# Optimization experiments

Hardware: AMD Instinct MI355X
Metric: run time of the kernel (lower is better)

The kernel has to match this reference:

```python
import jax, jax.numpy as jnp
import numpy as np

B = 4096
D = 512
N_I = 1000000
N_T = 1000000
GAMMA = 0.8
EPS = 1e-10
RHO_I = 8.0
RHO_T = 8.0
ETA_INIT = 1e-05
BETA_U = 0.5
GRAD_CLIP = 5.0
TAU_MIN, TAU_MAX = 0.005, 0.05
TAU_INIT = 0.01


def setup_inputs() -> dict:
    key = jax.random.key(0)
    k1, k2 = jax.random.split(key)
    img = jax.random.normal(k1, (B, D), jnp.float32)
    txt = jax.random.normal(k2, (B, D), jnp.float32)
    # CLIP-style L2-normalized features
    img = img / jnp.linalg.norm(img, axis=1, keepdims=True)
    txt = txt / jnp.linalg.norm(txt, axis=1, keepdims=True)
    return {
        "image_features": img,
        "text_features": txt,
        "s_I": jnp.zeros(N_I, jnp.float32),
        "s_T": jnp.zeros(N_T, jnp.float32),
        "b_I": jnp.zeros(N_I, jnp.float32),
        "b_T": jnp.zeros(N_T, jnp.float32),
        "u_I": jnp.zeros(N_I, jnp.float32),
        "u_T": jnp.zeros(N_T, jnp.float32),
        "tau_I": jnp.full((N_I,), TAU_INIT, jnp.float32),
        "tau_T": jnp.full((N_T,), TAU_INIT, jnp.float32),
        "image_ids": jnp.arange(B, dtype=jnp.int32),
        "text_ids": jnp.arange(B, dtype=jnp.int32),
        "epoch": 1,
    }


def reference(image_features, text_features, s_I, s_T, b_I, b_T, u_I, u_T,
              tau_I, tau_T, image_ids, text_ids, epoch):
    sg = jax.lax.stop_gradient
    sim = jnp.einsum('id,jd->ij', image_features, text_features)  # [B,B]
    diag = jnp.diagonal(sim)
    Bn = sim.shape[0]
    tau_img = tau_I[image_ids]  # [B]
    tau_txt = tau_T[text_ids]   # [B]
    image_diffs = sim - diag[:, None]
    text_diffs = sim - diag[None, :]
    # .detach() in the original -> stop_gradient here
    idt = sg(image_diffs / tau_img[:, None])
    tdt = sg(text_diffs / tau_txt[None, :])
    old_b_I = b_I[image_ids]
    old_b_T = b_T[text_ids]
    # running max for log-sum-exp stabilization
    b_I_row = jnp.maximum(idt.max(axis=1), old_b_I)
    b_T_col = jnp.maximum(tdt.max(axis=0), old_b_T)
    b_I_new = b_I.at[image_ids].set(b_I_row)
    b_T_new = b_T.at[text_ids].set(b_T_col)
    mask = 1.0 - jnp.eye(Bn, dtype=sim.dtype)
    exp_i = jnp.exp(idt - b_I_row[:, None]) * mask
    exp_t = jnp.exp(tdt - b_T_col[None, :]) * mask
    g_I = exp_i.sum(axis=1)
    g_T = exp_t.sum(axis=0)
    if epoch == 0:
        sI = g_I
        sT = g_T
    else:
        sI = (1.0 - GAMMA) * s_I[image_ids] * jnp.exp(old_b_I - b_I_row) + GAMMA * g_I
        sT = (1.0 - GAMMA) * s_T[text_ids] * jnp.exp(old_b_T - b_T_col) + GAMMA * g_T
    s_I_new = s_I.at[image_ids].set(sI)
    s_T_new = s_T.at[text_ids].set(sT)
    w_i = sg(exp_i / (sI[:, None] + EPS))
    w_t = sg(exp_t / (sT[None, :] + EPS))
    image_loss = (w_i * image_diffs).sum(axis=1)
    text_loss = (w_t * text_diffs).sum(axis=0)
    total_loss = image_loss.mean() + text_loss.mean()
    tw_i = jnp.log(sI / (Bn - 1)) + b_I_row + RHO_I - (w_i * idt).sum(axis=1)
    tw_t = jnp.log(sT / (Bn - 1)) + b_T_col + RHO_T - (w_t * tdt).sum(axis=0)
    # torch uses in-place clamp_ on a view, so the returned means are clipped
    tw_i = jnp.clip(tw_i, -GRAD_CLIP, GRAD_CLIP)
    tw_t = jnp.clip(tw_t, -GRAD_CLIP, GRAD_CLIP)
    u_I_val = (1.0 - BETA_U) * u_I[image_ids] + BETA_U * tw_i
    u_T_val = (1.0 - BETA_U) * u_T[text_ids] + BETA_U * tw_t
    u_I_new = u_I.at[image_ids].set(u_I_val)
    u_T_new = u_T.at[text_ids].set(u_T_val)
    tau_I_new = tau_I.at[image_ids].set(jnp.clip(tau_img - ETA_INIT * u_I_val, TAU_MIN, TAU_MAX))
    tau_T_new = tau_T.at[text_ids].set(jnp.clip(tau_txt - ETA_INIT * u_T_val, TAU_MIN, TAU_MAX))
    return (total_loss, tau_img.mean(), tau_txt.mean(), tw_i.mean(), tw_t.mean(),
            s_I_new, s_T_new, b_I_new, b_T_new, u_I_new, u_T_new, tau_I_new, tau_T_new)
```

## Files before the change

### kernel.cpp

```cpp
#include <hip/hip_runtime.h>

typedef unsigned short u16;
typedef unsigned int u32;

typedef __bf16 bf16x8 __attribute__((ext_vector_type(8)));
typedef float floatx4 __attribute__((ext_vector_type(4)));

__device__ __forceinline__ u16 f2bf(float f) {
    union { float f; u32 u; } c; c.f = f;
    u32 u = c.u;
    u32 r = u + 0x7FFFu + ((u >> 16) & 1u);
    return (u16)(r >> 16);
}
__device__ __forceinline__ float bf2f(u16 x) {
    union { u32 u; float f; } c; c.u = ((u32)x) << 16; return c.f;
}

__device__ __forceinline__ void comb(float& M, float& P0, float& P1,
                                     float m, float p0, float p1) {
    float nm = fmaxf(M, m);
    float s = __expf(M - nm), t = __expf(m - nm);
    P0 = P0 * s + p0 * t;
    P1 = P1 * s + p1 * t;
    M = nm;
}

__device__ __forceinline__ void dma16(const u16* g, u16* l) {
#if __has_builtin(__builtin_amdgcn_global_load_lds)
    __builtin_amdgcn_global_load_lds(
        (const __attribute__((address_space(1))) u32*)g,
        (__attribute__((address_space(3))) u32*)l, 16, 0, 0);
#else
    int lane = threadIdx.x & 63;
    *(uint4*)(l + lane * 8) = *(const uint4*)(g);
#endif
}

__global__ __launch_bounds__(256) void presplit(
    const float* __restrict__ a, const float* __restrict__ b,
    u16* __restrict__ Ah, u16* __restrict__ Al,
    u16* __restrict__ Bh, u16* __restrict__ Bl, int n,
    const float* __restrict__ tauI, const float* __restrict__ tauT,
    const int* __restrict__ img_ids, const int* __restrict__ txt_ids,
    float* __restrict__ taur, float* __restrict__ tauc) {
    if (blockIdx.y == 0 && blockIdx.x < 16) {
        int t = blockIdx.x * 256 + threadIdx.x;
        taur[t] = tauI[img_ids[t]];
        tauc[t] = tauT[txt_ids[t]];
    }
    const float* src = blockIdx.y ? b : a;
    u16* dh = blockIdx.y ? Bh : Ah;
    u16* dl = blockIdx.y ? Bl : Al;
    int i = (blockIdx.x * 256 + threadIdx.x) * 8;
    if (i >= n) return;
    float4 v0 = *(const float4*)&src[i];
    float4 v1 = *(const float4*)&src[i + 4];
    float xs[8] = {v0.x, v0.y, v0.z, v0.w, v1.x, v1.y, v1.z, v1.w};
    u16 h[8], l[8];
#pragma unroll
    for (int e = 0; e < 8; e++) {
        h[e] = f2bf(xs[e]);
        l[e] = f2bf(xs[e] - bf2f(h[e]));
    }
    *(uint4*)&dh[i] = *(uint4*)h;
    *(uint4*)&dl[i] = *(uint4*)l;
}

#define COPY_BLOCKS 2048

__global__ __launch_bounds__(256) void gemm_flash(
    const u16* __restrict__ Ah, const u16* __restrict__ Al,
    const u16* __restrict__ Bh, const u16* __restrict__ Bl,
    const float* __restrict__ taur, const float* __restrict__ tauc,
    float* __restrict__ rowpart, float* __restrict__ colpart,
    float* __restrict__ diag,
    const float* __restrict__ p0, const float* __restrict__ p1,
    const float* __restrict__ p2, const float* __restrict__ p3,
    const float* __restrict__ p4, const float* __restrict__ p5,
    const float* __restrict__ p6, const float* __restrict__ p7,
    float* __restrict__ out, long long n) {
    __shared__ __align__(16) u16 sAh[128 * 32];
    __shared__ __align__(16) u16 sAl[128 * 32];
    __shared__ __align__(16) u16 sBh[128 * 32];
    __shared__ __align__(16) u16 sBl[128 * 32];
    __shared__ float redbuf[1536];

    const int bid = blockIdx.x;
    if (bid >= 1024) {
        const int cb = bid - 1024;
        const float* srcs[8] = {p0, p1, p2, p3, p4, p5, p6, p7};
        const long long total = 8 * n;
        const long long G = (total - 3) >> 2;
        for (long long g = (long long)cb * 256 + threadIdx.x; g < G;
             g += (long long)COPY_BLOCKS * 256) {
            long long e = 3 + 4 * g;
            int k = (int)(e / n);
            long long bound = (long long)(k + 1) * n;
            float vv[4];
#pragma unroll
            for (int j = 0; j < 4; j++) {
                long long ee = e + j;
                int kk = (ee >= bound) ? k + 1 : k;
                vv[j] = srcs[kk][ee - (long long)kk * n];
            }
            float4 q = {vv[0], vv[1], vv[2], vv[3]};
            *(float4*)&out[5 + e] = q;
        }
        if (cb == 0) {
            int t = threadIdx.x;
            long long tail0 = 3 + 4 * G;
            int tcount = (int)(total - tail0);
            long long e = -1;
            if (t < 3) e = t;
            else if (t < 3 + tcount) e = tail0 + (t - 3);
            if (e >= 0) {
                int k = (int)(e / n);
                out[5 + e] = srcs[k][e - (long long)k * n];
            }
        }
        return;
    }

    const int tid  = threadIdx.x;
    const int wave = tid >> 6, lane = tid & 63;
    const int lr = lane & 15, quad = lane >> 4;
    const int waveM = wave >> 1, waveN = wave & 1;
    const int rowtile = bid >> 5, coltile = bid & 31;
    const int rowBase = rowtile * 128;
    const int colBase = coltile * 128;

    const int o0 = wave * 1024 + lane * 16;
    const int o1 = o0 + 4096;
    const int r0s = o0 >> 6, c0s = (o0 & 63) >> 1;
    const int r1s = o1 >> 6, c1s = (o1 & 63) >> 1;
    const int l0 = wave * 512;
    const int l1 = wave * 512 + 2048;

    floatx4 acc[4][4];
#pragma unroll
    for (int mi = 0; mi < 4; mi++)
#pragma unroll
        for (int ni = 0; ni < 4; ni++) acc[mi][ni] = (floatx4)0.0f;

    for (int k0 = 0; k0 < 512; k0 += 32) {
        __syncthreads();
        dma16(&Ah[(size_t)(rowBase + r0s) * 512 + k0 + c0s], sAh + l0);
        dma16(&Ah[(size_t)(rowBase + r1s) * 512 + k0 + c1s], sAh + l1);
        dma16(&Al[(size_t)(rowBase + r0s) * 512 + k0 + c0s], sAl + l0);
        dma16(&Al[(size_t)(rowBase + r1s) * 512 + k0 + c1s], sAl + l1);
        dma16(&Bh[(size_t)(colBase + r0s) * 512 + k0 + c0s], sBh + l0);
        dma16(&Bh[(size_t)(colBase + r1s) * 512 + k0 + c1s], sBh + l1);
        dma16(&Bl[(size_t)(colBase + r0s) * 512 + k0 + c0s], sBl + l0);
        dma16(&Bl[(size_t)(colBase + r1s) * 512 + k0 + c1s], sBl + l1);
        __syncthreads();

        bf16x8 afh[4], afl[4], bfh[4], bfl[4];
#pragma unroll
        for (int mi = 0; mi < 4; mi++) {
            int off = (waveM * 64 + mi * 16 + lr) * 32 + quad * 8;
            afh[mi] = *(const bf16x8*)&sAh[off];
            afl[mi] = *(const bf16x8*)&sAl[off];
        }
#pragma unroll
        for (int ni = 0; ni < 4; ni++) {
            int off = (waveN * 64 + ni * 16 + lr) * 32 + quad * 8;
            bfh[ni] = *(const bf16x8*)&sBh[off];
            bfl[ni] = *(const bf16x8*)&sBl[off];
        }
#pragma unroll
        for (int mi = 0; mi < 4; mi++)
#pragma unroll
            for (int ni = 0; ni < 4; ni++) {
                acc[mi][ni] = __builtin_amdgcn_mfma_f32_16x16x32_bf16(afh[mi], bfh[ni], acc[mi][ni], 0, 0, 0);
                acc[mi][ni] = __builtin_amdgcn_mfma_f32_16x16x32_bf16(afh[mi], bfl[ni], acc[mi][ni], 0, 0, 0);
                acc[mi][ni] = __builtin_amdgcn_mfma_f32_16x16x32_bf16(afl[mi], bfh[ni], acc[mi][ni], 0, 0, 0);
            }
    }


    if (rowtile == coltile && waveM == waveN) {
#pragma unroll
        for (int mi = 0; mi < 4; mi++)
#pragma unroll
            for (int r = 0; r < 4; r++)
                if (lr == quad * 4 + r)
                    diag[colBase + waveN * 64 + mi * 16 + lr] = acc[mi][mi][r];
    }

#pragma unroll
    for (int mi = 0; mi < 4; mi++) {
#pragma unroll
        for (int r = 0; r < 4; r++) {
            int row_local = waveM * 64 + mi * 16 + quad * 4 + r;
            float it = 1.0f / taur[rowBase + row_local];
            float M = -3.4e38f, P0 = 0.f, P1 = 0.f;
#pragma unroll
            for (int ni = 0; ni < 4; ni++) {
                float y = acc[mi][ni][r] * it;
                comb(M, P0, P1, y, 1.0f, y);
            }
#pragma unroll
            for (int mask = 1; mask <= 8; mask <<= 1) {
                float om = __shfl_xor(M, mask);
                float o0 = __shfl_xor(P0, mask);
                float o1 = __shfl_xor(P1, mask);
                comb(M, P0, P1, om, o0, o1);
            }
            if (lr == 0) {
                int x = (row_local * 2 + waveN) * 3;
                redbuf[x] = M; redbuf[x + 1] = P0; redbuf[x + 2] = P1;
            }
        }
    }

#pragma unroll
    for (int ni = 0; ni < 4; ni++) {
        int col_local = waveN * 64 + ni * 16 + lr;
        float it = 1.0f / tauc[colBase + col_local];
        float M = -3.4e38f, P0 = 0.f, P1 = 0.f;
#pragma unroll
        for (int mi = 0; mi < 4; mi++)
#pragma unroll
            for (int r = 0; r < 4; r++) {
                float y = acc[mi][ni][r] * it;
                comb(M, P0, P1, y, 1.0f, y);
            }
#pragma unroll
        for (int mask = 16; mask <= 32; mask <<= 1) {
            float om = __shfl_xor(M, mask);
            float o0 = __shfl_xor(P0, mask);
            float o1 = __shfl_xor(P1, mask);
            comb(M, P0, P1, om, o0, o1);
        }
        if (quad == 0) {
            int x = 768 + (col_local * 2 + waveM) * 3;
            redbuf[x] = M; redbuf[x + 1] = P0; redbuf[x + 2] = P1;
        }
    }
    __syncthreads();

    if (tid < 128) {
        int x = tid * 6;
        float M = redbuf[x], P0 = redbuf[x + 1], P1 = redbuf[x + 2];
        comb(M, P0, P1, redbuf[x + 3], redbuf[x + 4], redbuf[x + 5]);
        float* dst = &rowpart[(size_t)(rowBase + tid) * 96 + coltile * 3];
        dst[0] = M; dst[1] = P0; dst[2] = P1;
    } else {
        int c = tid - 128;
        int x = 768 + c * 6;
        float M = redbuf[x], P0 = redbuf[x + 1], P1 = redbuf[x + 2];
        comb(M, P0, P1, redbuf[x + 3], redbuf[x + 4], redbuf[x + 5]);
        float* dst = &colpart[(size_t)(colBase + c) * 96 + rowtile * 3];
        dst[0] = M; dst[1] = P0; dst[2] = P1;
    }
}

struct FinArgs {
    const float* rowpart; const float* colpart; const float* diag;
    const float* tauI; const float* sI; const float* bI; const float* uI;
    const float* tauT; const float* sT; const float* bT; const float* uT;
    const int* img_ids; const int* txt_ids; const int* epoch_p;
    float* out; float* rowbuf; long long n;
};

__global__ __launch_bounds__(256) void rows_final(FinArgs a) {
    int t = blockIdx.x * 256 + threadIdx.x;
    int side = t >> 12, i = t & 4095;
    const float* part   = side ? a.colpart : a.rowpart;
    const int*   ids    = side ? a.txt_ids : a.img_ids;
    const float* tau_in = side ? a.tauT : a.tauI;
    const float* s_in   = side ? a.sT   : a.sI;
    const float* b_in   = side ? a.bT   : a.bI;
    const float* u_in   = side ? a.uT   : a.uI;

    const float* p = part + (size_t)i * 96;
    float M = -3.4e38f, P0 = 0.f, P1 = 0.f;
#pragma unroll 4
    for (int k = 0; k < 32; k++)
        comb(M, P0, P1, p[3 * k], p[3 * k + 1], p[3 * k + 2]);

    const int id = ids[i];
    const float tau   = tau_in[id];
    const float old_b = b_in[id];
    const float old_s = s_in[id];
    const float old_u = u_in[id];
    const float y_ii  = a.diag[i] / tau;

    float b_row = fmaxf(M - y_ii, old_b);
    float e  = expf(M - y_ii - b_row);
    float S0 = P0 * e - expf(-b_row);
    float S1 = (P1 - y_ii * P0) * e;

    float g = S0;
    float sI = (*a.epoch_p == 0) ? g
             : 0.2f * old_s * expf(old_b - b_row) + 0.8f * g;
    float denom = sI + 1e-10f;
    float wsum = S1 / denom;
    float lossr = tau * wsum;
    float tw = logf(sI * (1.0f / 4095.0f)) + b_row + 8.0f - wsum;
    tw = fminf(fmaxf(tw, -5.0f), 5.0f);
    float uval = 0.5f * old_u + 0.5f * tw;
    float taun = fminf(fmaxf(tau - 1e-5f * uval, 0.005f), 0.05f);

    float* sect = a.out + 5;
    sect[(size_t)(0 + side) * (size_t)a.n + id] = sI;
    sect[(size_t)(2 + side) * (size_t)a.n + id] = b_row;
    sect[(size_t)(4 + side) * (size_t)a.n + id] = uval;
    sect[(size_t)(6 + side) * (size_t)a.n + id] = taun;

    a.rowbuf[(2 * side + 0) * 4096 + i] = lossr;
    a.rowbuf[(2 * side + 1) * 4096 + i] = tw;
}

__global__ __launch_bounds__(256) void scalars(
    const float* __restrict__ rows,
    const float* __restrict__ tau_I, const float* __restrict__ tau_T,
    const int* __restrict__ image_ids, const int* __restrict__ text_ids,
    float* __restrict__ out) {
    int tid = threadIdx.x;
    int lane = tid & 63, wv = tid >> 6;
    float a[6] = {0, 0, 0, 0, 0, 0};
    for (int e = tid; e < 4096; e += 256) {
        a[0] += rows[0 * 4096 + e];
        a[1] += rows[1 * 4096 + e];
        a[2] += rows[2 * 4096 + e];
        a[3] += rows[3 * 4096 + e];
        a[4] += tau_I[image_ids[e]];
        a[5] += tau_T[text_ids[e]];
    }
    __shared__ float sred[4][6];
#pragma unroll
    for (int k = 0; k < 6; k++)
        for (int o = 32; o > 0; o >>= 1) a[k] += __shfl_xor(a[k], o);
    if (lane == 0)
#pragma unroll
        for (int k = 0; k < 6; k++) sred[wv][k] = a[k];
    __syncthreads();
    if (tid == 0) {
#pragma unroll
        for (int k = 0; k < 6; k++)
            a[k] = sred[0][k] + sred[1][k] + sred[2][k] + sred[3][k];
        const float inv = 1.0f / 4096.0f;
        out[0] = (a[0] + a[2]) * inv;
        out[1] = a[4] * inv;
        out[2] = a[5] * inv;
        out[3] = a[1] * inv;
        out[4] = a[3] * inv;
    }
}

extern "C" void kernel_launch(void* const* d_in, const int* in_sizes, int n_in,
                              void* d_out, int out_size, void* d_ws, size_t ws_size,
                              hipStream_t stream) {
    const float* img   = (const float*)d_in[0];
    const float* txt   = (const float*)d_in[1];
    const float* s_I   = (const float*)d_in[2];
    const float* s_T   = (const float*)d_in[3];
    const float* b_I   = (const float*)d_in[4];
    const float* b_T   = (const float*)d_in[5];
    const float* u_I   = (const float*)d_in[6];
    const float* u_T   = (const float*)d_in[7];
    const float* tau_I = (const float*)d_in[8];
    const float* tau_T = (const float*)d_in[9];
    const int* image_ids = (const int*)d_in[10];
    const int* text_ids  = (const int*)d_in[11];
    const int* epoch     = (const int*)d_in[12];
    float* out = (float*)d_out;
    const long long n = in_sizes[2];
    const int nfeat = in_sizes[0];

    const size_t MB = 1024 * 1024;
    u16* Ah = (u16*)d_ws;
    u16* Al = Ah + (size_t)nfeat;
    u16* Bh = Al + (size_t)nfeat;
    u16* Bl = Bh + (size_t)nfeat;
    float* rowpart = (float*)((char*)d_ws + 16 * MB);
    float* colpart = (float*)((char*)d_ws + 18 * MB);
    float* diag    = (float*)((char*)d_ws + 20 * MB);
    float* taur    = (float*)((char*)d_ws + 20 * MB + 256 * 1024);
    float* tauc    = (float*)((char*)d_ws + 20 * MB + 512 * 1024);
    float* rows    = (float*)((char*)d_ws + 21 * MB);

    presplit<<<dim3((nfeat / 8 + 255) / 256, 2), 256, 0, stream>>>(
        img, txt, Ah, Al, Bh, Bl, nfeat,
        tau_I, tau_T, image_ids, text_ids, taur, tauc);

    gemm_flash<<<1024 + COPY_BLOCKS, 256, 0, stream>>>(
        Ah, Al, Bh, Bl, taur, tauc, rowpart, colpart, diag,
        s_I, s_T, b_I, b_T, u_I, u_T, tau_I, tau_T, out, n);

    FinArgs fa;
    fa.rowpart = rowpart; fa.colpart = colpart; fa.diag = diag;
    fa.tauI = tau_I; fa.sI = s_I; fa.bI = b_I; fa.uI = u_I;
    fa.tauT = tau_T; fa.sT = s_T; fa.bT = b_T; fa.uT = u_T;
    fa.img_ids = image_ids; fa.txt_ids = text_ids; fa.epoch_p = epoch;
    fa.out = out; fa.rowbuf = rows; fa.n = n;
    rows_final<<<32, 256, 0, stream>>>(fa);

    scalars<<<1, 256, 0, stream>>>(rows, tau_I, tau_T, image_ids, text_ids, out);
}
```

Baseline: 210.3 us.

## Use two-pass max-then-sum tile epilogue, alias LDS, and split copy per source array

The per-tile online softmax reduction, which called two exps per element and shuffled three values, becomes a max pass followed by one exp per element and plain sum shuffles. The reduction buffer now aliases the GEMM staging LDS, with a barrier added before reuse, to cut shared memory per block. The state-copy blocks are split so each group of 256 blocks copies one source array, which removes per-element division and array selection. The max-first form relies on positive tau so that scaling and max commute, and the copy mapping assumes COPY_BLOCKS is 2048, covering 8 arrays of 256 blocks each.

```diff
diff --git a/kernel.cpp b/kernel.cpp
--- a/kernel.cpp
+++ b/kernel.cpp
@@ -79,44 +79,33 @@
     const float* __restrict__ p4, const float* __restrict__ p5,
     const float* __restrict__ p6, const float* __restrict__ p7,
     float* __restrict__ out, long long n) {
-    __shared__ __align__(16) u16 sAh[128 * 32];
-    __shared__ __align__(16) u16 sAl[128 * 32];
-    __shared__ __align__(16) u16 sBh[128 * 32];
-    __shared__ __align__(16) u16 sBl[128 * 32];
-    __shared__ float redbuf[1536];
+    __shared__ __align__(16) u16 smem[4 * 128 * 32];
+    u16* sAh = smem;
+    u16* sAl = smem + 4096;
+    u16* sBh = smem + 8192;
+    u16* sBl = smem + 12288;
+    float* redbuf = (float*)smem;
 
     const int bid = blockIdx.x;
     if (bid >= 1024) {
         const int cb = bid - 1024;
+        const int k = cb >> 8, blk = cb & 255;
         const float* srcs[8] = {p0, p1, p2, p3, p4, p5, p6, p7};
-        const long long total = 8 * n;
-        const long long G = (total - 3) >> 2;
-        for (long long g = (long long)cb * 256 + threadIdx.x; g < G;
-             g += (long long)COPY_BLOCKS * 256) {
+        const float* src = srcs[k];
+        float* dst = out + 5 + (size_t)k * (size_t)n;
+        const long long G = (n - 3) >> 2;
+        for (long long g = (long long)blk * 256 + threadIdx.x; g < G;
+             g += 256 * 256) {
             long long e = 3 + 4 * g;
-            int k = (int)(e / n);
-            long long bound = (long long)(k + 1) * n;
-            float vv[4];
-#pragma unroll
-            for (int j = 0; j < 4; j++) {
-                long long ee = e + j;
-                int kk = (ee >= bound) ? k + 1 : k;
-                vv[j] = srcs[kk][ee - (long long)kk * n];
-            }
-            float4 q = {vv[0], vv[1], vv[2], vv[3]};
-            *(float4*)&out[5 + e] = q;
-        }
-        if (cb == 0) {
+            float4 q = {src[e], src[e + 1], src[e + 2], src[e + 3]};
+            *(float4*)&dst[e] = q;
+        }
+        if (blk == 0) {
             int t = threadIdx.x;
             long long tail0 = 3 + 4 * G;
-            int tcount = (int)(total - tail0);
-            long long e = -1;
-            if (t < 3) e = t;
-            else if (t < 3 + tcount) e = tail0 + (t - 3);
-            if (e >= 0) {
-                int k = (int)(e / n);
-                out[5 + e] = srcs[k][e - (long long)k * n];
-            }
+            int tcount = (int)(n - tail0);
+            if (t < 3) dst[t] = src[t];
+            else if (t < 3 + tcount) dst[tail0 + (t - 3)] = src[tail0 + (t - 3)];
         }
         return;
     }
@@ -176,6 +165,7 @@
                 acc[mi][ni] = __builtin_amdgcn_mfma_f32_16x16x32_bf16(afl[mi], bfh[ni], acc[mi][ni], 0, 0, 0);
             }
     }
+    __syncthreads();
 
 
     if (rowtile == coltile && waveM == waveN) {
@@ -192,19 +182,25 @@
 #pragma unroll
         for (int r = 0; r < 4; r++) {
             int row_local = waveM * 64 + mi * 16 + quad * 4 + r;
+            float vmax = fmaxf(fmaxf(acc[mi][0][r], acc[mi][1][r]),
+                               fmaxf(acc[mi][2][r], acc[mi][3][r]));
+#pragma unroll
+            for (int mask = 1; mask <= 8; mask <<= 1)
+                vmax = fmaxf(vmax, __shfl_xor(vmax, mask));
             float it = 1.0f / taur[rowBase + row_local];
-            float M = -3.4e38f, P0 = 0.f, P1 = 0.f;
+            float M = vmax * it;
+            float P0 = 0.f, P1 = 0.f;
 #pragma unroll
             for (int ni = 0; ni < 4; ni++) {
                 float y = acc[mi][ni][r] * it;
-                comb(M, P0, P1, y, 1.0f, y);
+                float e = __expf(y - M);
+                P0 += e;
+                P1 += y * e;
             }
 #pragma unroll
             for (int mask = 1; mask <= 8; mask <<= 1) {
-                float om = __shfl_xor(M, mask);
-                float o0 = __shfl_xor(P0, mask);
-                float o1 = __shfl_xor(P1, mask);
-                comb(M, P0, P1, om, o0, o1);
+                P0 += __shfl_xor(P0, mask);
+                P1 += __shfl_xor(P1, mask);
             }
             if (lr == 0) {
                 int x = (row_local * 2 + waveN) * 3;
@@ -216,21 +212,31 @@
 #pragma unroll
     for (int ni = 0; ni < 4; ni++) {
         int col_local = waveN * 64 + ni * 16 + lr;
+        float vmax = -3.4e38f;
+#pragma unroll
+        for (int mi = 0; mi < 4; mi++)
+            vmax = fmaxf(vmax,
+                fmaxf(fmaxf(acc[mi][ni][0], acc[mi][ni][1]),
+                      fmaxf(acc[mi][ni][2], acc[mi][ni][3])));
+#pragma unroll
+        for (int mask = 16; mask <= 32; mask <<= 1)
+            vmax = fmaxf(vmax, __shfl_xor(vmax, mask));
         float it = 1.0f / tauc[colBase + col_local];
-        float M = -3.4e38f, P0 = 0.f, P1 = 0.f;
+        float M = vmax * it;
+        float P0 = 0.f, P1 = 0.f;
 #pragma unroll
         for (int mi = 0; mi < 4; mi++)
 #pragma unroll
             for (int r = 0; r < 4; r++) {
                 float y = acc[mi][ni][r] * it;
-                comb(M, P0, P1, y, 1.0f, y);
+                float e = __expf(y - M);
+                P0 += e;
+                P1 += y * e;
             }
 #pragma unroll
         for (int mask = 16; mask <= 32; mask <<= 1) {
-            float om = __shfl_xor(M, mask);
-            float o0 = __shfl_xor(P0, mask);
-            float o1 = __shfl_xor(P1, mask);
-            comb(M, P0, P1, om, o0, o1);
+            P0 += __shfl_xor(P0, mask);
+            P1 += __shfl_xor(P1, mask);
         }
         if (quad == 0) {
             int x = 768 + (col_local * 2 + waveM) * 3;
```

After: 203.3 us. -3.4%, faster.
